# Optimization experiments

Hardware: AMD Instinct MI355X
Metric: run time of the kernel (lower is better)

Reference implementation:

```python
import jax, jax.numpy as jnp
import numpy as np

B, T, D, H, NL, V = 2, 2048, 512, 8, 4, 32000
HD = D // H
EPS = 1e-5


def _ln(x, g, b):
    mu = jnp.mean(x, axis=-1, keepdims=True)
    var = jnp.var(x, axis=-1, keepdims=True)
    return (x - mu) * jax.lax.rsqrt(var + EPS) * g + b


def setup_inputs() -> dict:
    key = jax.random.key(0)
    ks = jax.random.split(key, 16)
    f = lambda k, shp: jax.random.normal(k, shp, jnp.float32) * 0.02
    return {
        "token_ids": jax.random.randint(ks[0], (B, T), 0, V),
        "labels": jax.random.randint(ks[1], (B, T), 0, V),
        "tok_emb": f(ks[2], (V, D)),
        "pos_emb": f(ks[3], (T, D)),
        "Wq": f(ks[4], (NL, H, D, HD)),
        "Wk": f(ks[5], (NL, H, D, HD)),
        "Wv": f(ks[6], (NL, H, D, HD)),
        "Wo": f(ks[7], (NL, D, D)),
        "bo": jnp.zeros((NL, D), jnp.float32),
        "ln1_g": jnp.ones((NL, D), jnp.float32),
        "ln1_b": jnp.zeros((NL, D), jnp.float32),
        "ln2_g": jnp.ones((NL, D), jnp.float32),
        "ln2_b": jnp.zeros((NL, D), jnp.float32),
        "W1": f(ks[8], (NL, D, 4 * D)),
        "b1": jnp.zeros((NL, 4 * D), jnp.float32),
        "W2": f(ks[9], (NL, 4 * D, D)),
        "b2": jnp.zeros((NL, D), jnp.float32),
        "lnf_g": jnp.ones((D,), jnp.float32),
        "lnf_b": jnp.zeros((D,), jnp.float32),
        "Wp": f(ks[10], (D, V)),
        "bp": jnp.zeros((V,), jnp.float32),
    }


def reference(token_ids, labels, tok_emb, pos_emb, Wq, Wk, Wv, Wo, bo,
              ln1_g, ln1_b, ln2_g, ln2_b, W1, b1, W2, b2, lnf_g, lnf_b, Wp, bp):
    x = tok_emb[token_ids] + pos_emb[:T]            # (B, T, D)
    causal = jnp.tril(jnp.ones((T, T), bool))       # tril buffer
    scale = D ** -0.5                               # NOTE: source scales by dim_embed, not head_size
    for l in range(NL):
        xn = _ln(x, ln1_g[l], ln1_b[l])
        q = jnp.einsum('btd,hde->bhte', xn, Wq[l])  # (B, H, T, HD)
        k = jnp.einsum('btd,hde->bhte', xn, Wk[l])
        v = jnp.einsum('btd,hde->bhte', xn, Wv[l])
        w = jnp.einsum('bhte,bhse->bhts', q, k) * scale
        w = jnp.where(causal, w, -jnp.inf)
        w = jax.nn.softmax(w, axis=-1)
        o = jnp.einsum('bhts,bhse->bhte', w, v)     # (B, H, T, HD)
        o = o.transpose(0, 2, 1, 3).reshape(B, T, D)  # concat heads
        x = x + o @ Wo[l] + bo[l]
        xn = _ln(x, ln2_g[l], ln2_b[l])
        x = x + jax.nn.relu(xn @ W1[l] + b1[l]) @ W2[l] + b2[l]
    x = _ln(x, lnf_g, lnf_b)
    logits = x @ Wp + bp                            # (B, T, V)
    logits2d = logits.reshape(B * T, V)
    logp = jax.nn.log_softmax(logits2d, axis=-1)
    loss = -jnp.mean(logp[jnp.arange(B * T), labels.reshape(B * T)])
    return logits2d, loss
```

## Files before the change

### kernel.cpp

```cpp
#include <hip/hip_runtime.h>
#include <hip/hip_bf16.h>
#include <math.h>

#define B_ 2
#define T_ 2048
#define D_ 512
#define H_ 8
#define NL_ 4
#define V_ 32000
#define HD_ 64
#define BT_ (B_*T_)
#define EPS_ 1e-5f
#define SCALE_ 0.04419417382415922f
#define NEGBIG -1e30f

typedef __bf16 bf16x8 __attribute__((ext_vector_type(8)));
typedef float  f32x4  __attribute__((ext_vector_type(4)));

__device__ __forceinline__ unsigned short f2bf(float f) {
  union { float f; unsigned u; } v; v.f = f;
  unsigned r = v.u + 0x7fff + ((v.u >> 16) & 1);
  return (unsigned short)(r >> 16);
}

__device__ __forceinline__ void gl_lds16(const void* g, void* l) {
  __builtin_amdgcn_global_load_lds(
      (const __attribute__((address_space(1))) void*)g,
      (__attribute__((address_space(3))) void*)l, 16, 0, 0);
}

#define WAITVM(n) asm volatile("s_waitcnt vmcnt(" #n ")" ::: "memory")
#define WAITLG0   asm volatile("s_waitcnt lgkmcnt(0)" ::: "memory")

__global__ __launch_bounds__(256) void embed_kernel(
    const int* __restrict__ ids, const float* __restrict__ tok,
    const float* __restrict__ pos, float* __restrict__ x)
{
  int i = blockIdx.x * 256 + threadIdx.x;
  int d4 = i & (D_/4 - 1);
  int bt = i >> 7;
  int t  = bt & (T_ - 1);
  const float4 a = reinterpret_cast<const float4*>(tok + (size_t)ids[bt] * D_)[d4];
  const float4 p = reinterpret_cast<const float4*>(pos + (size_t)t * D_)[d4];
  float4 r; r.x = a.x + p.x; r.y = a.y + p.y; r.z = a.z + p.z; r.w = a.w + p.w;
  reinterpret_cast<float4*>(x)[i] = r;
}

__global__ __launch_bounds__(256) void ln_kernel(
    const float* __restrict__ x, const float* __restrict__ g,
    const float* __restrict__ b, unsigned short* __restrict__ out)
{
  int row  = blockIdx.x * 4 + (threadIdx.x >> 6);
  int lane = threadIdx.x & 63;
  const float4* xr = reinterpret_cast<const float4*>(x + (size_t)row * D_);
  float4 v0 = xr[lane], v1 = xr[lane + 64];
  float s = v0.x + v0.y + v0.z + v0.w + v1.x + v1.y + v1.z + v1.w;
  float q = v0.x*v0.x + v0.y*v0.y + v0.z*v0.z + v0.w*v0.w
          + v1.x*v1.x + v1.y*v1.y + v1.z*v1.z + v1.w*v1.w;
  #pragma unroll
  for (int off = 1; off < 64; off <<= 1) {
    s += __shfl_xor(s, off);
    q += __shfl_xor(q, off);
  }
  float mean = s * (1.0f / D_);
  float var  = q * (1.0f / D_) - mean * mean;
  float rs   = rsqrtf(var + EPS_);
  const float4* g4 = reinterpret_cast<const float4*>(g);
  const float4* b4 = reinterpret_cast<const float4*>(b);
  float4 gv0 = g4[lane], gv1 = g4[lane + 64];
  float4 bv0 = b4[lane], bv1 = b4[lane + 64];
  ushort4 p0, p1;
  p0.x = f2bf((v0.x - mean) * rs * gv0.x + bv0.x);
  p0.y = f2bf((v0.y - mean) * rs * gv0.y + bv0.y);
  p0.z = f2bf((v0.z - mean) * rs * gv0.z + bv0.z);
  p0.w = f2bf((v0.w - mean) * rs * gv0.w + bv0.w);
  p1.x = f2bf((v1.x - mean) * rs * gv1.x + bv1.x);
  p1.y = f2bf((v1.y - mean) * rs * gv1.y + bv1.y);
  p1.z = f2bf((v1.z - mean) * rs * gv1.z + bv1.z);
  p1.w = f2bf((v1.w - mean) * rs * gv1.w + bv1.w);
  unsigned short* orow = out + (size_t)row * D_;
  *reinterpret_cast<ushort4*>(orow + lane * 4)       = p0;
  *reinterpret_cast<ushort4*>(orow + 256 + lane * 4) = p1;
}

__global__ __launch_bounds__(256) void transpose_cast(
    const float* __restrict__ src, unsigned short* __restrict__ dst,
    int C, int R, long sstride, long dstride)
{
  src += (size_t)blockIdx.z * sstride;
  dst += (size_t)blockIdx.z * dstride;
  __shared__ float t[32][33];
  int r0 = blockIdx.x * 32, c0 = blockIdx.y * 32;
  int tx = threadIdx.x & 31, ty = threadIdx.x >> 5;
  #pragma unroll
  for (int i = 0; i < 4; i++)
    t[ty + i*8][tx] = src[(size_t)(r0 + ty + i*8) * C + c0 + tx];
  __syncthreads();
  #pragma unroll
  for (int i = 0; i < 4; i++)
    dst[(size_t)(c0 + ty + i*8) * R + r0 + tx] = f2bf(t[tx][ty + i*8]);
}

__global__ __launch_bounds__(256) void qkvw_transpose(
    const float* __restrict__ Wq, const float* __restrict__ Wk,
    const float* __restrict__ Wv, unsigned short* __restrict__ dst)
{
  int z = blockIdx.z; int l = z / 24; int rem = z % 24; int mat = rem >> 3; int h = rem & 7;
  const float* W = (mat == 0 ? Wq : (mat == 1 ? Wk : Wv)) + ((size_t)(l * 8 + h)) * D_ * HD_;
  unsigned short* d = dst + ((size_t)l * 1536 + mat * 512 + h * 64) * D_;
  __shared__ float t[32][33];
  int d0 = blockIdx.x * 32, e0 = blockIdx.y * 32;
  int tx = threadIdx.x & 31, ty = threadIdx.x >> 5;
  #pragma unroll
  for (int i = 0; i < 4; i++)
    t[ty + i*8][tx] = W[(size_t)(d0 + ty + i*8) * HD_ + e0 + tx];
  __syncthreads();
  #pragma unroll
  for (int i = 0; i < 4; i++)
    d[(size_t)(e0 + ty + i*8) * D_ + d0 + tx] = f2bf(t[tx][ty + i*8]);
}

__global__ __launch_bounds__(512, 4) void gemm_logits(
    const unsigned short* __restrict__ A,
    const unsigned short* __restrict__ Bt,
    int K, const float* __restrict__ bias,
    float* __restrict__ outF, int ldc,
    float2* __restrict__ ms, int npan)
{
  __shared__ __align__(16) char smem[73728];
  unsigned short* Abase = (unsigned short*)smem;
  unsigned short* Bbase = (unsigned short*)(smem + 24576);
  float* E = (float*)smem;

  const int tid = threadIdx.x;
  const int lane = tid & 63;
  const int lr = lane & 15, g = lane >> 4;
  const int wv = tid >> 6, wm = wv >> 2, wn = wv & 3;

  const int gx = gridDim.x;
  int id = blockIdx.y * gx + blockIdx.x;
  const int nwg = gx * gridDim.y;
  if ((nwg & 7) == 0) { const int q = nwg >> 3; id = (id & 7) * q + (id >> 3); }
  const int bm = (id % gx) * 128, bn = (id / gx) * 256, bnp = id / gx;

  const int schk = (lane & 3) ^ ((lane >> 3) & 3);
  const unsigned short* Ab = A  + (size_t)(bm + wv*16 + (lane >> 2)) * K + schk * 8;
  const unsigned short* Bb = Bt + (size_t)(bn + wv*16 + (lane >> 2)) * K + schk * 8;

#define STAGEL(s, sl)                                                       \
  { const int kof_ = (s) * 32;                                              \
    gl_lds16(Ab + kof_,                 Abase + (sl)*4096 + wv*512);        \
    gl_lds16(Bb + kof_,                 Bbase + (sl)*8192 + wv*512);        \
    gl_lds16(Bb + (size_t)128*K + kof_, Bbase + (sl)*8192 + 4096 + wv*512); }

  f32x4 acc[4][4];
  #pragma unroll
  for (int m = 0; m < 4; m++)
    #pragma unroll
    for (int n = 0; n < 4; n++)
      acc[m][n] = (f32x4){0.f, 0.f, 0.f, 0.f};

  const int nt = K >> 5;
  STAGEL(0, 0); STAGEL(1, 1);

  const int slotx = (g ^ ((lr >> 1) & 3)) << 3;

  for (int t = 0; t < nt; ++t) {
    const int s = t + 2;
    const int st = t % 3;
    __builtin_amdgcn_sched_barrier(0);
    if      (s < nt)  { const int ss = s % 3; STAGEL(s, ss); WAITVM(6); }
    else if (s == nt) { WAITVM(3); }
    else              { WAITVM(0); }
    __builtin_amdgcn_sched_barrier(0);
    __builtin_amdgcn_s_barrier();
    __builtin_amdgcn_sched_barrier(0);

    const unsigned short* Ac = Abase + st*4096;
    const unsigned short* Bc = Bbase + st*8192;
    bf16x8 af[4], bfr[4];
    #pragma unroll
    for (int m = 0; m < 4; m++)
      af[m] = *reinterpret_cast<const bf16x8*>(&Ac[(wm*64 + m*16 + lr) * 32 + slotx]);
    #pragma unroll
    for (int n = 0; n < 4; n++)
      bfr[n] = *reinterpret_cast<const bf16x8*>(&Bc[(wn*64 + n*16 + lr) * 32 + slotx]);
    __builtin_amdgcn_s_setprio(1);
    #pragma unroll
    for (int m = 0; m < 4; m++)
      #pragma unroll
      for (int n = 0; n < 4; n++)
        acc[m][n] = __builtin_amdgcn_mfma_f32_16x16x32_bf16(af[m], bfr[n], acc[m][n], 0, 0, 0);
    __builtin_amdgcn_s_setprio(0);
    __builtin_amdgcn_sched_barrier(0);
    __builtin_amdgcn_s_barrier();
  }
#undef STAGEL

  #pragma unroll
  for (int n = 0; n < 4; n++) {
    const float bv = bias ? bias[bn + wn*64 + n*16 + lr] : 0.f;
    #pragma unroll
    for (int m = 0; m < 4; m++)
      #pragma unroll
      for (int r = 0; r < 4; r++)
        acc[m][n][r] += bv;
  }

  if (ms) {
    #pragma unroll
    for (int m = 0; m < 4; m++) {
      float vmax[4] = {NEGBIG, NEGBIG, NEGBIG, NEGBIG};
      #pragma unroll
      for (int n = 0; n < 4; n++)
        #pragma unroll
        for (int r = 0; r < 4; r++)
          vmax[r] = fmaxf(vmax[r], acc[m][n][r]);
      #pragma unroll
      for (int r = 0; r < 4; r++) {
        #pragma unroll
        for (int off = 1; off < 16; off <<= 1)
          vmax[r] = fmaxf(vmax[r], __shfl_xor(vmax[r], off));
      }
      float vsum[4] = {0.f, 0.f, 0.f, 0.f};
      #pragma unroll
      for (int n = 0; n < 4; n++)
        #pragma unroll
        for (int r = 0; r < 4; r++)
          vsum[r] += __expf(acc[m][n][r] - vmax[r]);
      #pragma unroll
      for (int r = 0; r < 4; r++) {
        #pragma unroll
        for (int off = 1; off < 16; off <<= 1)
          vsum[r] += __shfl_xor(vsum[r], off);
      }
      if (lr == 0) {
        #pragma unroll
        for (int r = 0; r < 4; r++)
          ms[(size_t)(bm + wm*64 + m*16 + g*4 + r) * npan + bnp*4 + wn] =
              make_float2(vmax[r], vsum[r]);
      }
    }
  }

  #pragma unroll
  for (int c = 0; c < 2; ++c) {
    __syncthreads();
    if (wm == c) {
      #pragma unroll
      for (int m = 0; m < 4; m++)
        #pragma unroll
        for (int n = 0; n < 4; n++)
          #pragma unroll
          for (int r = 0; r < 4; r++)
            E[(m*16 + g*4 + r) * 260 + wn*64 + n*16 + lr] = acc[m][n][r];
    }
    __syncthreads();
    #pragma unroll
    for (int rep = 0; rep < 8; rep++) {
      const int row = rep*8 + wv;
      f32x4 v = *reinterpret_cast<const f32x4*>(&E[row*260 + lane*4]);
      __builtin_nontemporal_store(
          v, reinterpret_cast<f32x4*>(&outF[(size_t)(bm + c*64 + row) * ldc + bn + lane*4]));
    }
  }
}

template<int BM_T, int BN_T, int WM, int WN>
__global__ __launch_bounds__(256) void gemm_pipe(
    const unsigned short* __restrict__ A,
    const unsigned short* __restrict__ Bt,
    int K,
    const float* __restrict__ bias,
    const float* __restrict__ resid,
    float* __restrict__ outF,
    unsigned short* __restrict__ outH,
    int ldc, int relu)
{
  constexpr int BKp = 64;
  constexpr int ALOADS = BM_T / 32;
  constexpr int BLOADS = BN_T / 32;
  constexpr int LOADS  = ALOADS + BLOADS;
  constexpr int MR = BM_T / (16 * WM);
  constexpr int NR = BN_T / (16 * WN);
  __shared__ __align__(16) unsigned short As[2][BM_T * BKp];
  __shared__ __align__(16) unsigned short Bs[2][BN_T * BKp];

  const int tid = threadIdx.x;
  const int lane = tid & 63, wv = tid >> 6;
  const int lr = lane & 15, g = lane >> 4;

  const int gx = gridDim.x;
  int id = blockIdx.y * gx + blockIdx.x;
  const int nwg = gx * gridDim.y;
  if ((nwg & 7) == 0) {
    const int q = nwg >> 3;
    id = (id & 7) * q + (id >> 3);
  }
  const int bm = (id % gx) * BM_T, bn = (id / gx) * BN_T;

  const int m0w = (wv / WN) * (BM_T / WM);
  const int n0w = (wv % WN) * (BN_T / WN);

  const int srow = wv*8 + (lane >> 3);
  const int schk = (lane & 7) ^ (lane >> 3);
  const unsigned short* Ab = A  + (size_t)(bm + srow) * K + schk * 8;
  const unsigned short* Bb = Bt + (size_t)(bn + srow) * K + schk * 8;

#define STAGEP(s, sl)                                                           \
  { const int kof_ = (s) * BKp;                                                 \
    _Pragma("unroll")                                                           \
    for (int i_ = 0; i_ < ALOADS; ++i_)                                         \
      gl_lds16(Ab + (size_t)(i_*32)*K + kof_, As[sl] + i_*2048 + wv*512);       \
    _Pragma("unroll")                                                           \
    for (int i_ = 0; i_ < BLOADS; ++i_)                                         \
      gl_lds16(Bb + (size_t)(i_*32)*K + kof_, Bs[sl] + i_*2048 + wv*512); }

  f32x4 acc[MR][NR];
  #pragma unroll
  for (int m = 0; m < MR; m++)
    #pragma unroll
    for (int n = 0; n < NR; n++)
      acc[m][n] = (f32x4){0.f, 0.f, 0.f, 0.f};

  const int nt = K >> 6;
  STAGEP(0, 0);

  for (int t = 0; t < nt; ++t) {
    __builtin_amdgcn_sched_barrier(0);
    if (t + 1 < nt) {
      STAGEP(t + 1, (t + 1) & 1);
      if constexpr (LOADS == 4) WAITVM(4);
      else if constexpr (LOADS == 6) WAITVM(6);
      else WAITVM(8);
    } else {
      WAITVM(0);
    }
    __builtin_amdgcn_sched_barrier(0);
    __builtin_amdgcn_s_barrier();
    __builtin_amdgcn_sched_barrier(0);

    const unsigned short* Ac = As[t & 1];
    const unsigned short* Bc = Bs[t & 1];
    #pragma unroll
    for (int kk = 0; kk < 2; ++kk) {
      const int sl = ((kk*4 + g) ^ (lr & 7)) << 3;
      bf16x8 af[MR], bfr[NR];
      #pragma unroll
      for (int m = 0; m < MR; m++)
        af[m] = *reinterpret_cast<const bf16x8*>(&Ac[(m0w + m*16 + lr) * BKp + sl]);
      #pragma unroll
      for (int n = 0; n < NR; n++)
        bfr[n] = *reinterpret_cast<const bf16x8*>(&Bc[(n0w + n*16 + lr) * BKp + sl]);
      __builtin_amdgcn_s_setprio(1);
      #pragma unroll
      for (int m = 0; m < MR; m++)
        #pragma unroll
        for (int n = 0; n < NR; n++)
          acc[m][n] = __builtin_amdgcn_mfma_f32_16x16x32_bf16(af[m], bfr[n], acc[m][n], 0, 0, 0);
      __builtin_amdgcn_s_setprio(0);
    }
    __builtin_amdgcn_sched_barrier(0);
    __builtin_amdgcn_s_barrier();
  }
#undef STAGEP

  const int cr = g * 4;
  const int cc = lr;
  #pragma unroll
  for (int m = 0; m < MR; m++) {
    #pragma unroll
    for (int n = 0; n < NR; n++) {
      int row = bm + m0w + m*16 + cr;
      int col = bn + n0w + n*16 + cc;
      f32x4 a = acc[m][n];
      #pragma unroll
      for (int r = 0; r < 4; r++) {
        float v = a[r];
        if (bias)  v += bias[col];
        if (resid) v += resid[(size_t)(row + r) * ldc + col];
        if (relu)  v = fmaxf(v, 0.f);
        if (outF)  outF[(size_t)(row + r) * ldc + col] = v;
        if (outH)  outH[(size_t)(row + r) * ldc + col] = f2bf(v);
      }
    }
  }
}

__global__ __launch_bounds__(512) void attn_mfma(
    const unsigned short* __restrict__ qkv,
    unsigned short* __restrict__ o,
    float* __restrict__ Opart,
    float2* __restrict__ ml)
{
  __shared__ __align__(16) unsigned short Ks[2][64*64];
  __shared__ __align__(16) unsigned short Vt[2][64*64];
  __shared__ __align__(16) unsigned short Ps[8][16*64];

  static const unsigned char ord[24] = {7,22,23,20,21,6,18,19,16,17,5,14,15,12,13,4,10,11,8,9,3,2,1,0};
  const int slot = ord[blockIdx.x];
  const int bh = blockIdx.y, bb = bh >> 3, hh = bh & 7;
  int qb, it0, itn, half;
  if (slot < 8) { qb = slot; it0 = 0; itn = 2*qb + 2; half = -1; }
  else { const int p = slot - 8; qb = 8 + (p >> 1); half = p & 1;
         const int nh = qb + 1; it0 = half * nh; itn = nh; }

  const int tid = threadIdx.x, lane = tid & 63, wv = tid >> 6;
  const int lr = lane & 15, g = lane >> 4;

  const unsigned short* qp = qkv + ((size_t)(bb*T_ + qb*128))*1536 + hh*64;
  const unsigned short* kp = qkv + ((size_t)bb*T_)*1536 + 512  + hh*64;
  const unsigned short* vp = qkv + ((size_t)bb*T_)*1536 + 1024 + hh*64;

  bf16x8 qf[2];
  qf[0] = *reinterpret_cast<const bf16x8*>(qp + (size_t)(wv*16 + lr)*1536 + g*8);
  qf[1] = *reinterpret_cast<const bf16x8*>(qp + (size_t)(wv*16 + lr)*1536 + 32 + g*8);

  const int krow = wv*8 + (lane >> 3);
  const int khb  = (lane & 7) ^ (lane >> 3);

#define STAGE_K(s0_, buf_)                                           \
  gl_lds16(kp + (size_t)((s0_)*64 + krow)*1536 + khb*8,              \
           (void*)(Ks[buf_] + wv*512));

  uint4 uvr;
#define LOAD_V(s0_)                                                  \
  uvr = *reinterpret_cast<const uint4*>(                             \
      vp + (size_t)((s0_)*64 + lane)*1536 + wv*8);

  f32x4 ov[4];
  #pragma unroll
  for (int n = 0; n < 4; n++) ov[n] = (f32x4){0.f, 0.f, 0.f, 0.f};
  float mrow[4] = {NEGBIG, NEGBIG, NEGBIG, NEGBIG};
  float lrow[4] = {0.f, 0.f, 0.f, 0.f};

  STAGE_K(it0, 0);
  LOAD_V(it0);

  for (int ii = 0; ii < itn; ++ii) {
    const int s0 = it0 + ii;
    const int cur = ii & 1;
    WAITVM(0);
    __builtin_amdgcn_sched_barrier(0);
    {
      union { uint4 v; unsigned short e[8]; } uv; uv.v = uvr;
      #pragma unroll
      for (int j = 0; j < 8; j++)
        Vt[cur][(wv*8 + j)*64 + (((lane >> 3) ^ j) << 3) + (lane & 7)] = uv.e[j];
    }
    WAITLG0;
    __builtin_amdgcn_sched_barrier(0);
    __builtin_amdgcn_s_barrier();
    __builtin_amdgcn_sched_barrier(0);

    if (ii + 1 < itn) {
      STAGE_K(s0 + 1, cur ^ 1);
      LOAD_V(s0 + 1);
    }

    f32x4 sf[4];
    #pragma unroll
    for (int n = 0; n < 4; n++) sf[n] = (f32x4){0.f, 0.f, 0.f, 0.f};
    __builtin_amdgcn_s_setprio(1);
    #pragma unroll
    for (int kk = 0; kk < 2; kk++) {
      #pragma unroll
      for (int n = 0; n < 4; n++) {
        const bf16x8 kf = *reinterpret_cast<const bf16x8*>(
            &Ks[cur][(n*16 + lr)*64 + (((kk*4 + g) ^ (lr & 7)) << 3)]);
        sf[n] = __builtin_amdgcn_mfma_f32_16x16x32_bf16(qf[kk], kf, sf[n], 0, 0, 0);
      }
    }
    __builtin_amdgcn_s_setprio(0);

    float sv[4][4];
    #pragma unroll
    for (int n = 0; n < 4; n++)
      #pragma unroll
      for (int r = 0; r < 4; r++) {
        const int kvg = s0*64 + n*16 + lr;
        const int qg  = qb*128 + wv*16 + g*4 + r;
        sv[n][r] = (kvg > qg) ? NEGBIG : sf[n][r] * SCALE_;
      }

    float aa[4];
    #pragma unroll
    for (int r = 0; r < 4; r++) {
      float pm = fmaxf(fmaxf(sv[0][r], sv[1][r]), fmaxf(sv[2][r], sv[3][r]));
      pm = fmaxf(pm, __shfl_xor(pm, 1));
      pm = fmaxf(pm, __shfl_xor(pm, 2));
      pm = fmaxf(pm, __shfl_xor(pm, 4));
      pm = fmaxf(pm, __shfl_xor(pm, 8));
      float mn = fmaxf(mrow[r], pm);
      aa[r] = __expf(mrow[r] - mn);
      mrow[r] = mn;
    }
    float rs[4] = {0.f, 0.f, 0.f, 0.f};
    #pragma unroll
    for (int n = 0; n < 4; n++)
      #pragma unroll
      for (int r = 0; r < 4; r++) {
        float p = __expf(sv[n][r] - mrow[r]);
        rs[r] += p;
        Ps[wv][(g*4 + r)*64 + ((((n << 1) + (lr >> 3)) ^ ((g*4 + r) & 7)) << 3) + (lr & 7)] = f2bf(p);
      }
    #pragma unroll
    for (int r = 0; r < 4; r++) {
      float s = rs[r];
      s += __shfl_xor(s, 1); s += __shfl_xor(s, 2);
      s += __shfl_xor(s, 4); s += __shfl_xor(s, 8);
      lrow[r] = lrow[r]*aa[r] + s;
    }
    #pragma unroll
    for (int n = 0; n < 4; n++)
      #pragma unroll
      for (int r = 0; r < 4; r++)
        ov[n][r] *= aa[r];

    __builtin_amdgcn_s_setprio(1);
    #pragma unroll
    for (int kk = 0; kk < 2; kk++) {
      const bf16x8 pf = *reinterpret_cast<const bf16x8*>(
          &Ps[wv][lr*64 + (((kk*4 + g) ^ (lr & 7)) << 3)]);
      #pragma unroll
      for (int n = 0; n < 4; n++) {
        const bf16x8 vf = *reinterpret_cast<const bf16x8*>(
            &Vt[cur][(n*16 + lr)*64 + (((kk*4 + g) ^ (lr & 7)) << 3)]);
        ov[n] = __builtin_amdgcn_mfma_f32_16x16x32_bf16(pf, vf, ov[n], 0, 0, 0);
      }
    }
    __builtin_amdgcn_s_setprio(0);
    __builtin_amdgcn_sched_barrier(0);
    __builtin_amdgcn_s_barrier();
  }
#undef STAGE_K
#undef LOAD_V

  if (half < 0) {
    #pragma unroll
    for (int r = 0; r < 4; r++) {
      float inv = 1.0f / lrow[r];
      size_t row = (size_t)(bb*T_ + qb*128 + wv*16 + g*4 + r);
      #pragma unroll
      for (int n = 0; n < 4; n++)
        o[row*D_ + hh*64 + n*16 + lr] = f2bf(ov[n][r] * inv);
    }
  } else {
    const int blk = bh*8 + (qb - 8);
    float* Od = Opart + ((size_t)blk*2 + half)*128*64;
    #pragma unroll
    for (int r = 0; r < 4; r++) {
      const int rloc = wv*16 + g*4 + r;
      #pragma unroll
      for (int n = 0; n < 4; n++)
        Od[rloc*64 + n*16 + lr] = ov[n][r];
      if (lr == 0)
        ml[((size_t)blk*2 + half)*128 + rloc] = make_float2(mrow[r], lrow[r]);
    }
  }
}

__global__ __launch_bounds__(256) void attn_merge(
    const float* __restrict__ Opart, const float2* __restrict__ ml,
    unsigned short* __restrict__ o)
{
  const int blk = blockIdx.x;
  const int bh = blk >> 3, qb = (blk & 7) + 8;
  const int bb = bh >> 3, hh = bh & 7;
  const int tid = threadIdx.x;
  const int row = tid >> 1, ch = (tid & 1) * 32;
  const float* O0 = Opart + ((size_t)blk*2 + 0)*128*64;
  const float* O1 = Opart + ((size_t)blk*2 + 1)*128*64;
  const float2 a = ml[(size_t)blk*2*128 + row];
  const float2 b = ml[((size_t)blk*2 + 1)*128 + row];
  const float M  = fmaxf(a.x, b.x);
  const float e0 = __expf(a.x - M), e1 = __expf(b.x - M);
  const float inv = 1.0f / (a.y*e0 + b.y*e1);
  unsigned short* orow = o + ((size_t)(bb*T_ + qb*128 + row))*D_ + hh*64 + ch;
  #pragma unroll
  for (int c = 0; c < 32; c += 4) {
    f32x4 v0 = *reinterpret_cast<const f32x4*>(&O0[row*64 + ch + c]);
    f32x4 v1 = *reinterpret_cast<const f32x4*>(&O1[row*64 + ch + c]);
    ushort4 pk;
    pk.x = f2bf((v0[0]*e0 + v1[0]*e1) * inv);
    pk.y = f2bf((v0[1]*e0 + v1[1]*e1) * inv);
    pk.z = f2bf((v0[2]*e0 + v1[2]*e1) * inv);
    pk.w = f2bf((v0[3]*e0 + v1[3]*e1) * inv);
    *reinterpret_cast<ushort4*>(&orow[c]) = pk;
  }
}

__global__ __launch_bounds__(256) void loss_merge_kernel(
    const float2* __restrict__ ms, const float* __restrict__ logits,
    const int* __restrict__ labels, float* __restrict__ rowloss, int npan)
{
  const int tid = threadIdx.x, lane = tid & 63, wid = tid >> 6;
  const int row = blockIdx.x * 4 + wid;
  float M = NEGBIG, S = 0.f;
  const float2* p = ms + (size_t)row * npan;
  for (int i = lane; i < npan; i += 64) {
    float2 e = p[i];
    float Mn = fmaxf(M, e.x);
    S = S * __expf(M - Mn) + e.y * __expf(e.x - Mn);
    M = Mn;
  }
  #pragma unroll
  for (int off = 1; off < 64; off <<= 1) {
    float Mo = __shfl_xor(M, off), So = __shfl_xor(S, off);
    float Mn = fmaxf(M, Mo);
    S = S * __expf(M - Mn) + So * __expf(Mo - Mn);
    M = Mn;
  }
  if (lane == 0)
    rowloss[row] = logits[(size_t)row * V_ + labels[row]] - M - logf(S);
}

__global__ __launch_bounds__(256) void loss_final_kernel(
    const float* __restrict__ rowloss, float* __restrict__ out)
{
  __shared__ float red[4];
  const int tid = threadIdx.x, lane = tid & 63, wid = tid >> 6;
  float s = 0.f;
  for (int i = tid; i < BT_; i += 256) s += rowloss[i];
  #pragma unroll
  for (int off = 1; off < 64; off <<= 1) s += __shfl_xor(s, off);
  if (lane == 0) red[wid] = s;
  __syncthreads();
  if (tid == 0) out[0] = -(red[0] + red[1] + red[2] + red[3]) * (1.0f / BT_);
}

extern "C" void kernel_launch(void* const* d_in, const int* in_sizes, int n_in,
                              void* d_out, int out_size, void* d_ws, size_t ws_size,
                              hipStream_t stream)
{
  (void)in_sizes; (void)n_in; (void)out_size; (void)ws_size;
  const int*   ids    = (const int*)d_in[0];
  const int*   labels = (const int*)d_in[1];
  const float* tok    = (const float*)d_in[2];
  const float* pos    = (const float*)d_in[3];
  const float* Wq     = (const float*)d_in[4];
  const float* Wk     = (const float*)d_in[5];
  const float* Wv     = (const float*)d_in[6];
  const float* Wo     = (const float*)d_in[7];
  const float* bo     = (const float*)d_in[8];
  const float* ln1g   = (const float*)d_in[9];
  const float* ln1b   = (const float*)d_in[10];
  const float* ln2g   = (const float*)d_in[11];
  const float* ln2b   = (const float*)d_in[12];
  const float* W1     = (const float*)d_in[13];
  const float* b1     = (const float*)d_in[14];
  const float* W2     = (const float*)d_in[15];
  const float* b2     = (const float*)d_in[16];
  const float* lnfg   = (const float*)d_in[17];
  const float* lnfb   = (const float*)d_in[18];
  const float* Wp     = (const float*)d_in[19];
  const float* bp     = (const float*)d_in[20];

  float* out = (float*)d_out;
  char* base = (char*)d_ws;
  float*          x       = (float*)(base + 0);
  unsigned short* xn      = (unsigned short*)(base + 8388608);
  float*          rowloss = (float*)(base + 12582912);
  unsigned short* WqkvT   = (unsigned short*)(base + 12599296);
  unsigned short* W1T     = (unsigned short*)(base + 18890752);
  unsigned short* W2T     = (unsigned short*)(base + 27279360);
  unsigned short* WoT     = (unsigned short*)(base + 35667968);
  unsigned short* qkvh    = (unsigned short*)(base + 37765120);
  unsigned short* ob      = (unsigned short*)(base + 50348032);
  unsigned short* h1      = (unsigned short*)(base + 54542336);
  float*          Opart   = (float*)(base + 54542336);
  float2*         mlbuf   = (float2*)(base + 62930944);
  unsigned short* WpT     = (unsigned short*)(base + 37765120);
  float2*         msbuf   = (float2*)(base + 12599296);

  embed_kernel<<<BT_ * D_ / 4 / 256, 256, 0, stream>>>(ids, tok, pos, x);

  qkvw_transpose<<<dim3(16, 2, 96), 256, 0, stream>>>(Wq, Wk, Wv, WqkvT);
  transpose_cast<<<dim3(16, 64, 4), 256, 0, stream>>>(W1, W1T, 2048, 512, 1048576, 1048576);
  transpose_cast<<<dim3(64, 16, 4), 256, 0, stream>>>(W2, W2T, 512, 2048, 1048576, 1048576);
  transpose_cast<<<dim3(16, 16, 4), 256, 0, stream>>>(Wo, WoT, 512, 512, 262144, 262144);

  for (int l = 0; l < NL_; l++) {
    ln_kernel<<<BT_ / 4, 256, 0, stream>>>(x, ln1g + l * D_, ln1b + l * D_, xn);
    gemm_pipe<64,64,2,2><<<dim3(64, 24), 256, 0, stream>>>(
        xn, WqkvT + (size_t)l * 1536 * 512, 512, nullptr, nullptr, nullptr, qkvh, 1536, 0);
    attn_mfma<<<dim3(24, B_ * H_), 512, 0, stream>>>(qkvh, ob, Opart, mlbuf);
    attn_merge<<<128, 256, 0, stream>>>(Opart, mlbuf, ob);
    gemm_pipe<64,64,2,2><<<dim3(64, 8), 256, 0, stream>>>(
        ob, WoT + (size_t)l * 512 * 512, 512, bo + l * D_, x, x, nullptr, D_, 0);
    ln_kernel<<<BT_ / 4, 256, 0, stream>>>(x, ln2g + l * D_, ln2b + l * D_, xn);
    gemm_pipe<64,64,2,2><<<dim3(64, 32), 256, 0, stream>>>(
        xn, W1T + (size_t)l * 2048 * 512, 512, b1 + l * 4 * D_, nullptr, nullptr, h1, 4 * D_, 1);
    gemm_pipe<64,64,2,2><<<dim3(64, 8), 256, 0, stream>>>(
        h1, W2T + (size_t)l * 512 * 2048, 2048, b2 + l * D_, x, x, nullptr, D_, 0);
  }

  transpose_cast<<<dim3(16, 1000, 1), 256, 0, stream>>>(Wp, WpT, 32000, 512, 0, 0);
  ln_kernel<<<BT_ / 4, 256, 0, stream>>>(x, lnfg, lnfb, xn);
  gemm_logits<<<dim3(32, 125), 512, 0, stream>>>(
      xn, WpT, 512, bp, out, V_, msbuf, 500);

  loss_merge_kernel<<<BT_ / 4, 256, 0, stream>>>(msbuf, out, labels, rowloss, 500);
  loss_final_kernel<<<1, 256, 0, stream>>>(rowloss, out + (size_t)BT_ * V_);
}
```

Baseline: 886.3 us.

## Skip lazy softmax rescale, remap logits GEMM tiles per XCD, raise attention occupancy

Attention now rescales the running max, sum and output accumulator only when some row's new block max exceeds the stored max by more than a threshold, checked with a wavefront ballot. Otherwise it keeps the stale max, which avoids exp and multiply work per tile but lets exponentials grow by up to e^8 before correction. The logits GEMM replaces its generic XCD swizzle with a hard-coded mapping that gives each XCD a contiguous range of vocab panels, aiming for better L2 reuse of the weight panels. The attention kernel also gets a min-blocks launch bound of 4, which can force register spills.

New measurement: 885.8 us. No clear change (-0.1%).

```diff
diff --git a/kernel.cpp b/kernel.cpp
--- a/kernel.cpp
+++ b/kernel.cpp
@@ -137,11 +137,12 @@
   const int lr = lane & 15, g = lane >> 4;
   const int wv = tid >> 6, wm = wv >> 2, wn = wv & 3;
 
-  const int gx = gridDim.x;
-  int id = blockIdx.y * gx + blockIdx.x;
-  const int nwg = gx * gridDim.y;
-  if ((nwg & 7) == 0) { const int q = nwg >> 3; id = (id & 7) * q + (id >> 3); }
-  const int bm = (id % gx) * 128, bn = (id / gx) * 256, bnp = id / gx;
+  const int id0 = blockIdx.y * gridDim.x + blockIdx.x;
+  const int xcd = id0 & 7, j = id0 >> 3;
+  int p, bxn;
+  if (j < 480) { p = xcd * 15 + (j >> 5); bxn = j & 31; }
+  else { const int k = xcd * 20 + (j - 480); p = 120 + (k >> 5); bxn = k & 31; }
+  const int bm = bxn * 128, bn = p * 256, bnp = p;
 
   const int schk = (lane & 3) ^ ((lane >> 3) & 3);
   const unsigned short* Ab = A  + (size_t)(bm + wv*16 + (lane >> 2)) * K + schk * 8;
@@ -387,7 +388,7 @@
   }
 }
 
-__global__ __launch_bounds__(512) void attn_mfma(
+__global__ __launch_bounds__(512, 4) void attn_mfma(
     const unsigned short* __restrict__ qkv,
     unsigned short* __restrict__ o,
     float* __restrict__ Opart,
@@ -483,7 +484,8 @@
         sv[n][r] = (kvg > qg) ? NEGBIG : sf[n][r] * SCALE_;
       }
 
-    float aa[4];
+    float pmv[4];
+    bool need = false;
     #pragma unroll
     for (int r = 0; r < 4; r++) {
       float pm = fmaxf(fmaxf(sv[0][r], sv[1][r]), fmaxf(sv[2][r], sv[3][r]));
@@ -491,9 +493,19 @@
       pm = fmaxf(pm, __shfl_xor(pm, 2));
       pm = fmaxf(pm, __shfl_xor(pm, 4));
       pm = fmaxf(pm, __shfl_xor(pm, 8));
-      float mn = fmaxf(mrow[r], pm);
-      aa[r] = __expf(mrow[r] - mn);
-      mrow[r] = mn;
+      pmv[r] = pm;
+      need |= (pm > mrow[r] + 8.0f);
+    }
+    if (__ballot(need)) {
+      #pragma unroll
+      for (int r = 0; r < 4; r++) {
+        float mn = fmaxf(mrow[r], pmv[r]);
+        float aa = __expf(mrow[r] - mn);
+        mrow[r] = mn;
+        lrow[r] *= aa;
+        #pragma unroll
+        for (int n = 0; n < 4; n++) ov[n][r] *= aa;
+      }
     }
     float rs[4] = {0.f, 0.f, 0.f, 0.f};
     #pragma unroll
@@ -509,13 +521,8 @@
       float s = rs[r];
       s += __shfl_xor(s, 1); s += __shfl_xor(s, 2);
       s += __shfl_xor(s, 4); s += __shfl_xor(s, 8);
-      lrow[r] = lrow[r]*aa[r] + s;
-    }
-    #pragma unroll
-    for (int n = 0; n < 4; n++)
-      #pragma unroll
-      for (int r = 0; r < 4; r++)
-        ov[n][r] *= aa[r];
+      lrow[r] += s;
+    }
 
     __builtin_amdgcn_s_setprio(1);
     #pragma unroll
```
